# Kernel optimization log

Hardware: AMD Instinct MI355X
Metric: run time of the kernel (lower is better)

## Reference

```python
import math
import jax, jax.numpy as jnp
import numpy as np

EMBED = 1024
INTERNAL = 1024  # EMBED // downsample_rate(=1)
HEADS = 16


def setup_inputs() -> dict:
    key = jax.random.key(0)
    ks = jax.random.split(key, 11)
    b, n, m = 2, 2048, 2048
    s = 1.0 / math.sqrt(EMBED)
    inp = {
        "q": jax.random.normal(ks[0], (b, n, EMBED), jnp.float32),
        "k": jax.random.normal(ks[1], (b, m, EMBED), jnp.float32),
        "v": jax.random.normal(ks[2], (b, m, EMBED), jnp.float32),
        # Linear params (torch Linear: y = x @ W.T + b); store as [in, out].
        "Wq": jax.random.normal(ks[3], (EMBED, INTERNAL), jnp.float32) * s,
        "bq": jax.random.normal(ks[4], (INTERNAL,), jnp.float32) * s,
        "Wk": jax.random.normal(ks[5], (EMBED, INTERNAL), jnp.float32) * s,
        "bk": jax.random.normal(ks[6], (INTERNAL,), jnp.float32) * s,
        "Wv": jax.random.normal(ks[7], (EMBED, INTERNAL), jnp.float32) * s,
        "bv": jax.random.normal(ks[8], (INTERNAL,), jnp.float32) * s,
        "Wo": jax.random.normal(ks[9], (INTERNAL, EMBED), jnp.float32) * s,
        "bo": jax.random.normal(ks[10], (EMBED,), jnp.float32) * s,
    }
    return inp


def _split_heads(x):  # [b, n, c] -> [b, h, n, c/h]
    b, n, c = x.shape
    return x.reshape(b, n, HEADS, c // HEADS).transpose(0, 2, 1, 3)


def reference(q, k, v, Wq, bq, Wk, bk, Wv, bv, Wo, bo):
    qh = _split_heads(q @ Wq + bq)
    kh = _split_heads(k @ Wk + bk)
    vh = _split_heads(v @ Wv + bv)
    c_per_head = kh.shape[-1]
    attn = jnp.einsum("bhnc,bhmc->bhnm", qh, kh) / math.sqrt(c_per_head)
    attn = jax.nn.softmax(attn, axis=-1)
    out = jnp.einsum("bhnm,bhmc->bhnc", attn, vh)
    b, h, n, ch = out.shape
    out = out.transpose(0, 2, 1, 3).reshape(b, n, h * ch)
    return out @ Wo + bo
```

## Files before the change

### kernel.cpp

```cpp
#include <hip/hip_runtime.h>

#define EMBED 1024
#define HEADS 16
#define DHEAD 64
#define BATCH 2
#define SEQ 2048
#define ROWS (BATCH*SEQ)
#define SZA (ROWS*EMBED)
#define SW (EMBED*EMBED)

typedef _Float16 f16;
typedef __attribute__((ext_vector_type(2))) __fp16 h16x2;
typedef __attribute__((ext_vector_type(4))) _Float16 f16x4;
typedef __attribute__((ext_vector_type(8))) _Float16 f16x8;
typedef __attribute__((ext_vector_type(4))) float f32x4;

__device__ __forceinline__ void gld16(const f16* g, f16* lds) {
  __builtin_amdgcn_global_load_lds(
      (const __attribute__((address_space(1))) void*)g,
      (__attribute__((address_space(3))) void*)lds, 16, 0, 0);
}

__global__ __launch_bounds__(256) void pre_kernel(
    const float* __restrict__ q, const float* __restrict__ k,
    const float* __restrict__ v, f16* __restrict__ qc,
    f16* __restrict__ kc, f16* __restrict__ vc,
    const float* __restrict__ w0, const float* __restrict__ w1,
    const float* __restrict__ w2, const float* __restrict__ w3,
    f16* __restrict__ o0, f16* __restrict__ o1,
    f16* __restrict__ o2, f16* __restrict__ o3) {
  __shared__ float tile[32][33];
  const int y = blockIdx.y;
  if (y < 3) {
    const float* in = y == 0 ? q : y == 1 ? k : v;
    f16* out       = y == 0 ? qc : y == 1 ? kc : vc;
    int i = blockIdx.x * 256 + threadIdx.x;
    float4 f = ((const float4* __restrict__)in)[i];
    union { f16 h[4]; short4 s4; } u;
    u.h[0] = (f16)f.x; u.h[1] = (f16)f.y; u.h[2] = (f16)f.z; u.h[3] = (f16)f.w;
    ((short4* __restrict__)out)[i] = u.s4;
    return;
  }
  const int x = blockIdx.x;
  const int z = x >> 10, by = (x >> 5) & 31, bx = x & 31;
  const float* in = z == 0 ? w0 : z == 1 ? w1 : z == 2 ? w2 : w3;
  f16* out       = z == 0 ? o0 : z == 1 ? o1 : z == 2 ? o2 : o3;
  int tx = threadIdx.x & 31, ty = threadIdx.x >> 5;
  #pragma unroll
  for (int i = 0; i < 32; i += 8)
    tile[ty + i][tx] = in[(by*32 + ty + i)*EMBED + bx*32 + tx];
  __syncthreads();
  #pragma unroll
  for (int i = 0; i < 32; i += 8)
    out[(bx*32 + ty + i)*EMBED + by*32 + tx] = (f16)tile[tx][ty + i];
}

__global__ __launch_bounds__(256) void gemm3_kernel(
    const f16* __restrict__ qc, const f16* __restrict__ kc, const f16* __restrict__ vc,
    const f16* __restrict__ Wqt, const f16* __restrict__ Wkt, const f16* __restrict__ Wvt,
    const float* __restrict__ bq, const float* __restrict__ bk, const float* __restrict__ bv,
    f16* __restrict__ Qp, f16* __restrict__ Kp, f16* __restrict__ Vtg) {
  __shared__ __align__(16) f16 As[128*32];
  __shared__ __align__(16) f16 Bs[128*32];
  const int z = blockIdx.y;
  const f16 *A, *Bt; const float* bias; f16* C;
  int mbase, nbase, N, biasrow;
  if (z == 0)      { A=qc;  Bt=Wqt; bias=bq; C=Qp;  mbase=(blockIdx.x&31)*128; nbase=(blockIdx.x>>5)*128; N=EMBED; biasrow=0; }
  else if (z == 1) { A=kc;  Bt=Wkt; bias=bk; C=Kp;  mbase=(blockIdx.x&31)*128; nbase=(blockIdx.x>>5)*128; N=EMBED; biasrow=0; }
  else             { A=Wvt; Bt=vc;  bias=bv; C=Vtg; mbase=(blockIdx.x&7)*128;  nbase=(blockIdx.x>>3)*128; N=ROWS;  biasrow=1; }
  const int K = EMBED;
  const int tid = threadIdx.x;
  const int wave = tid >> 6, lane = tid & 63;
  const int lg = lane >> 4, lr = lane & 15;
  const int wm = (wave >> 1) * 64, wn = (wave & 1) * 64;
  const int sr = lane >> 2;
  const int sc = ((lane & 3) ^ ((lane >> 3) & 3)) * 8;
  const f16* gA0 = A  + (size_t)(mbase + wave*16 + sr)*K + sc;
  const f16* gA1 = A  + (size_t)(mbase + 64 + wave*16 + sr)*K + sc;
  const f16* gB0 = Bt + (size_t)(nbase + wave*16 + sr)*K + sc;
  const f16* gB1 = Bt + (size_t)(nbase + 64 + wave*16 + sr)*K + sc;
  f16* lA0 = &As[(wave*16)*32];
  f16* lA1 = &As[(64 + wave*16)*32];
  f16* lB0 = &Bs[(wave*16)*32];
  f16* lB1 = &Bs[(64 + wave*16)*32];
  const int csw = (lg ^ ((lr >> 1) & 3)) * 8;
  f32x4 acc[4][4] = {};
  for (int k0 = 0; k0 < K; k0 += 32) {
    __syncthreads();
    gld16(gA0 + k0, lA0);
    gld16(gA1 + k0, lA1);
    gld16(gB0 + k0, lB0);
    gld16(gB1 + k0, lB1);
    __syncthreads();
    f16x8 af[4], bf[4];
    #pragma unroll
    for (int mt = 0; mt < 4; mt++)
      af[mt] = *(const f16x8*)&As[(wm + mt*16 + lr)*32 + csw];
    #pragma unroll
    for (int nt = 0; nt < 4; nt++)
      bf[nt] = *(const f16x8*)&Bs[(wn + nt*16 + lr)*32 + csw];
    #pragma unroll
    for (int mt = 0; mt < 4; mt++)
      #pragma unroll
      for (int nt = 0; nt < 4; nt++)
        acc[mt][nt] = __builtin_amdgcn_mfma_f32_16x16x32_f16(af[mt], bf[nt], acc[mt][nt], 0, 0, 0);
  }
  #pragma unroll
  for (int mt = 0; mt < 4; mt++)
    #pragma unroll
    for (int nt = 0; nt < 4; nt++)
      #pragma unroll
      for (int i = 0; i < 4; i++) {
        int row = mbase + wm + mt*16 + lg*4 + i;
        int col = nbase + wn + nt*16 + lr;
        float val = acc[mt][nt][i] + (biasrow ? bias[row] : bias[col]);
        if (z == 0) val *= 0.18033688011f;
        C[(size_t)row*N + col] = (f16)val;
      }
}

__global__ __launch_bounds__(256) void gemmo_kernel(
    const f16* __restrict__ A, const f16* __restrict__ Bt,
    const float* __restrict__ bias, float* __restrict__ Cf) {
  __shared__ __align__(16) f16 As[128*32];
  __shared__ __align__(16) f16 Bs[64*32];
  const int K = EMBED, N = EMBED;
  const int tid = threadIdx.x;
  const int wave = tid >> 6, lane = tid & 63;
  const int lg = lane >> 4, lr = lane & 15;
  const int mbase = blockIdx.x * 128, nbase = blockIdx.y * 64;
  const int wm = (wave >> 1) * 64, wn = (wave & 1) * 32;
  const int sr = wave*16 + (lane >> 2);
  const int sc = ((lane & 3) ^ ((lane >> 3) & 3)) * 8;
  const f16* gA0 = A  + (size_t)(mbase + sr)*K + sc;
  const f16* gA1 = A  + (size_t)(mbase + 64 + sr)*K + sc;
  const f16* gB  = Bt + (size_t)(nbase + sr)*K + sc;
  f16* lA0 = &As[(wave*16)*32];
  f16* lA1 = &As[(64 + wave*16)*32];
  f16* lB  = &Bs[(wave*16)*32];
  const int csw = (lg ^ ((lr >> 1) & 3)) * 8;
  f32x4 acc[4][2] = {};
  for (int k0 = 0; k0 < K; k0 += 32) {
    __syncthreads();
    gld16(gA0 + k0, lA0);
    gld16(gA1 + k0, lA1);
    gld16(gB  + k0, lB);
    __syncthreads();
    f16x8 af[4], bf[2];
    #pragma unroll
    for (int mt = 0; mt < 4; mt++)
      af[mt] = *(const f16x8*)&As[(wm + mt*16 + lr)*32 + csw];
    #pragma unroll
    for (int nt = 0; nt < 2; nt++)
      bf[nt] = *(const f16x8*)&Bs[(wn + nt*16 + lr)*32 + csw];
    #pragma unroll
    for (int mt = 0; mt < 4; mt++)
      #pragma unroll
      for (int nt = 0; nt < 2; nt++)
        acc[mt][nt] = __builtin_amdgcn_mfma_f32_16x16x32_f16(af[mt], bf[nt], acc[mt][nt], 0, 0, 0);
  }
  #pragma unroll
  for (int mt = 0; mt < 4; mt++)
    #pragma unroll
    for (int nt = 0; nt < 2; nt++)
      #pragma unroll
      for (int i = 0; i < 4; i++) {
        int row = mbase + wm + mt*16 + lg*4 + i;
        int col = nbase + wn + nt*16 + lr;
        Cf[(size_t)row*N + col] = acc[mt][nt][i] + bias[col];
      }
}

__global__ __launch_bounds__(256, 1) void attn_kernel(
    const f16* __restrict__ Qp, const f16* __restrict__ Kp,
    const f16* __restrict__ Vt, f16* __restrict__ Ob) {
  __shared__ __align__(16) f16 Ks[2*4096];
  __shared__ __align__(16) f16 Vs[2*4096];
  const int tid = threadIdx.x;
  const int wave = tid >> 6, lane = tid & 63;
  const int lg = lane >> 4, lr = lane & 15;
  const int gid = blockIdx.x;
  const int bh  = (gid & 7)*4 + ((gid >> 3) & 3);
  const int qblk = gid >> 5;
  const int h = bh & 15, b = bh >> 4;
  const int q0 = qblk*256 + wave*64;
  const f16* Qh = Qp + (size_t)b*SEQ*EMBED + h*DHEAD;
  const f16* Kh = Kp + (size_t)b*SEQ*EMBED + h*DHEAD;
  const f16* Vh = Vt + (size_t)h*DHEAD*ROWS + (size_t)b*SEQ;

  const f16* kst[2]; const f16* vst[2]; f16* kdst[2]; f16* vdst[2];
  #pragma unroll
  for (int m = 0; m < 2; m++) {
    int sgrp = m*4 + wave;
    int srow = sgrp*8 + (lane >> 3);
    int sch  = (lane & 7) ^ (srow & 7);
    int prow = ((srow>>5)&1)*32 + ((srow>>4)&1)*4 + ((srow>>2)&3)*8 + (srow&3);
    kst[m] = Kh + (size_t)prow*EMBED + sch*8;
    vst[m] = Vh + (size_t)srow*ROWS + sch*8;
    kdst[m] = &Ks[sgrp*512];
    vdst[m] = &Vs[sgrp*512];
  }

  f16x8 qf[4][2];
  #pragma unroll
  for (int qb = 0; qb < 4; qb++)
    #pragma unroll
    for (int ds = 0; ds < 2; ds++)
      qf[qb][ds] = *(const f16x8*)&Qh[(size_t)(q0 + qb*16 + lr)*EMBED + ds*32 + lg*8];

  const int c0 = ((lg)     ^ (lr & 7)) * 8;
  const int c1 = ((4 + lg) ^ (lr & 7)) * 8;

  f32x4 o[4][4] = {};
  f32x4 lacc[4] = {};
  const f32x4 NEG8 = {-8.f, -8.f, -8.f, -8.f};
  f16x8 onesf;
  #pragma unroll
  for (int i = 0; i < 8; i++) onesf[i] = (f16)1.0f;

  gld16(kst[0], kdst[0]);
  gld16(kst[1], kdst[1]);
  gld16(vst[0], vdst[0]);
  gld16(vst[1], vdst[1]);
  __syncthreads();

  for (int t = 0; t < 32; ++t) {
    const int bo = (t & 1) * 4096;
    if (t < 31) {
      const int po = 4096 - bo;
      const size_t kt = (size_t)(t + 1) * 64;
      gld16(kst[0] + kt*EMBED, kdst[0] + po);
      gld16(kst[1] + kt*EMBED, kdst[1] + po);
      gld16(vst[0] + kt, vdst[0] + po);
      gld16(vst[1] + kt, vdst[1] + po);
    }

    f16x8 ka[4][2], va[4][2];
    #pragma unroll
    for (int nb = 0; nb < 4; nb++) {
      ka[nb][0] = *(const f16x8*)&Ks[bo + (nb*16 + lr)*64 + c0];
      ka[nb][1] = *(const f16x8*)&Ks[bo + (nb*16 + lr)*64 + c1];
    }
    #pragma unroll
    for (int dm = 0; dm < 4; dm++) {
      va[dm][0] = *(const f16x8*)&Vs[bo + (dm*16 + lr)*64 + c0];
      va[dm][1] = *(const f16x8*)&Vs[bo + (dm*16 + lr)*64 + c1];
    }

    #pragma unroll
    for (int qb = 0; qb < 4; qb++) {
      f32x4 s[4];
      __builtin_amdgcn_s_setprio(1);
      #pragma unroll
      for (int nb = 0; nb < 4; nb++) {
        f32x4 z = __builtin_amdgcn_mfma_f32_16x16x32_f16(ka[nb][0], qf[qb][0], NEG8, 0, 0, 0);
        s[nb] = __builtin_amdgcn_mfma_f32_16x16x32_f16(ka[nb][1], qf[qb][1], z, 0, 0, 0);
      }
      __builtin_amdgcn_s_setprio(0);

      float p[4][4];
      #pragma unroll
      for (int nb = 0; nb < 4; nb++)
        #pragma unroll
        for (int i = 0; i < 4; i++)
          p[nb][i] = __builtin_amdgcn_exp2f(s[nb][i]);
      union { f16x8 v; h16x2 h2[4]; } u0, u1;
      u0.h2[0] = __builtin_amdgcn_cvt_pkrtz(p[0][0], p[0][1]);
      u0.h2[1] = __builtin_amdgcn_cvt_pkrtz(p[0][2], p[0][3]);
      u0.h2[2] = __builtin_amdgcn_cvt_pkrtz(p[1][0], p[1][1]);
      u0.h2[3] = __builtin_amdgcn_cvt_pkrtz(p[1][2], p[1][3]);
      u1.h2[0] = __builtin_amdgcn_cvt_pkrtz(p[2][0], p[2][1]);
      u1.h2[1] = __builtin_amdgcn_cvt_pkrtz(p[2][2], p[2][3]);
      u1.h2[2] = __builtin_amdgcn_cvt_pkrtz(p[3][0], p[3][1]);
      u1.h2[3] = __builtin_amdgcn_cvt_pkrtz(p[3][2], p[3][3]);
      const f16x8 pf0 = u0.v, pf1 = u1.v;

      __builtin_amdgcn_s_setprio(1);
      #pragma unroll
      for (int dm = 0; dm < 4; dm++)
        o[dm][qb] = __builtin_amdgcn_mfma_f32_16x16x32_f16(va[dm][0], pf0, o[dm][qb], 0, 0, 0);
      lacc[qb] = __builtin_amdgcn_mfma_f32_16x16x32_f16(onesf, pf0, lacc[qb], 0, 0, 0);
      #pragma unroll
      for (int dm = 0; dm < 4; dm++)
        o[dm][qb] = __builtin_amdgcn_mfma_f32_16x16x32_f16(va[dm][1], pf1, o[dm][qb], 0, 0, 0);
      lacc[qb] = __builtin_amdgcn_mfma_f32_16x16x32_f16(onesf, pf1, lacc[qb], 0, 0, 0);
      __builtin_amdgcn_s_setprio(0);
    }

    __syncthreads();
  }

  const float inv[4] = { 1.f / lacc[0][0], 1.f / lacc[1][0],
                         1.f / lacc[2][0], 1.f / lacc[3][0] };

  #pragma unroll
  for (int qb = 0; qb < 4; qb++) {
    const size_t rowb = (size_t)(b*SEQ + q0 + qb*16 + lr)*EMBED + h*DHEAD;
    #pragma unroll
    for (int dm = 0; dm < 4; dm++) {
      f16x4 w;
      #pragma unroll
      for (int i = 0; i < 4; i++) w[i] = (f16)(o[dm][qb][i] * inv[qb]);
      *(f16x4*)&Ob[rowb + dm*16 + 4*lg] = w;
    }
  }
}

extern "C" void kernel_launch(void* const* d_in, const int* in_sizes, int n_in,
                              void* d_out, int out_size, void* d_ws, size_t ws_size,
                              hipStream_t stream) {
  (void)in_sizes; (void)n_in; (void)out_size; (void)ws_size;
  const float* q  = (const float*)d_in[0];
  const float* k  = (const float*)d_in[1];
  const float* v  = (const float*)d_in[2];
  const float* Wq = (const float*)d_in[3];
  const float* bq = (const float*)d_in[4];
  const float* Wk = (const float*)d_in[5];
  const float* bk = (const float*)d_in[6];
  const float* Wv = (const float*)d_in[7];
  const float* bv = (const float*)d_in[8];
  const float* Wo = (const float*)d_in[9];
  const float* bo = (const float*)d_in[10];
  float* out = (float*)d_out;

  f16* w   = (f16*)d_ws;
  f16* qc  = w;
  f16* kc  = qc + SZA;
  f16* vc  = kc + SZA;
  f16* Qp  = vc + SZA;
  f16* Kp  = Qp + SZA;
  f16* Vtg = Kp + SZA;
  f16* Ob  = Vtg + SZA;
  f16* Wqt = Ob + SZA;
  f16* Wkt = Wqt + SW;
  f16* Wvt = Wkt + SW;
  f16* Wot = Wvt + SW;

  dim3 pg(4096, 4);
  pre_kernel<<<pg, 256, 0, stream>>>(q, k, v, qc, kc, vc,
                                     Wq, Wk, Wv, Wo, Wqt, Wkt, Wvt, Wot);
  dim3 g3(256, 3);
  gemm3_kernel<<<g3, 256, 0, stream>>>(qc, kc, vc, Wqt, Wkt, Wvt, bq, bk, bv, Qp, Kp, Vtg);
  attn_kernel<<<256, 256, 0, stream>>>(Qp, Kp, Vtg, Ob);
  dim3 go(ROWS/128, EMBED/64);
  gemmo_kernel<<<go, 256, 0, stream>>>(Ob, Wot, bo, out);
}
```

Before: 235.6 us.

## Split attention key dimension across wave pairs and double the grid

Each block now covers 128 query rows with four waves, where two waves share each 64-query slab and each handles half of every 64-key tile. Their partial outputs and row sums are combined through shared memory at the end. The grid grows from 256 to 512 blocks and launch bounds allow two blocks per CU, aiming to fill the 256 CUs better and hide latency. The cost is that K/V tiles are loaded twice as often per query, plus an extra reduction step and register pressure limits at two blocks per CU.

Result: faster. 210.7 us (-10.6%).

```diff
diff --git a/kernel.cpp b/kernel.cpp
--- a/kernel.cpp
+++ b/kernel.cpp
@@ -171,19 +171,21 @@
       }
 }
 
-__global__ __launch_bounds__(256, 1) void attn_kernel(
+__global__ __launch_bounds__(256, 2) void attn_kernel(
     const f16* __restrict__ Qp, const f16* __restrict__ Kp,
     const f16* __restrict__ Vt, f16* __restrict__ Ob) {
   __shared__ __align__(16) f16 Ks[2*4096];
   __shared__ __align__(16) f16 Vs[2*4096];
+  __shared__ float lred[2][4][64];
   const int tid = threadIdx.x;
   const int wave = tid >> 6, lane = tid & 63;
   const int lg = lane >> 4, lr = lane & 15;
+  const int qw = wave >> 1, kw = wave & 1;
   const int gid = blockIdx.x;
   const int bh  = (gid & 7)*4 + ((gid >> 3) & 3);
   const int qblk = gid >> 5;
   const int h = bh & 15, b = bh >> 4;
-  const int q0 = qblk*256 + wave*64;
+  const int q0 = qblk*128 + qw*64;
   const f16* Qh = Qp + (size_t)b*SEQ*EMBED + h*DHEAD;
   const f16* Kh = Kp + (size_t)b*SEQ*EMBED + h*DHEAD;
   const f16* Vh = Vt + (size_t)h*DHEAD*ROWS + (size_t)b*SEQ;
@@ -210,6 +212,7 @@
 
   const int c0 = ((lg)     ^ (lr & 7)) * 8;
   const int c1 = ((4 + lg) ^ (lr & 7)) * 8;
+  const int cv = kw ? c1 : c0;
 
   f32x4 o[4][4] = {};
   f32x4 lacc[4] = {};
@@ -224,6 +227,7 @@
   gld16(vst[1], vdst[1]);
   __syncthreads();
 
+  #pragma unroll 2
   for (int t = 0; t < 32; ++t) {
     const int bo = (t & 1) * 4096;
     if (t < 31) {
@@ -235,73 +239,86 @@
       gld16(vst[1] + kt, vdst[1] + po);
     }
 
-    f16x8 ka[4][2], va[4][2];
-    #pragma unroll
-    for (int nb = 0; nb < 4; nb++) {
-      ka[nb][0] = *(const f16x8*)&Ks[bo + (nb*16 + lr)*64 + c0];
-      ka[nb][1] = *(const f16x8*)&Ks[bo + (nb*16 + lr)*64 + c1];
+    f16x8 ka[2][2], va[4];
+    #pragma unroll
+    for (int n = 0; n < 2; n++) {
+      const int nb = 2*kw + n;
+      ka[n][0] = *(const f16x8*)&Ks[bo + (nb*16 + lr)*64 + c0];
+      ka[n][1] = *(const f16x8*)&Ks[bo + (nb*16 + lr)*64 + c1];
     }
     #pragma unroll
-    for (int dm = 0; dm < 4; dm++) {
-      va[dm][0] = *(const f16x8*)&Vs[bo + (dm*16 + lr)*64 + c0];
-      va[dm][1] = *(const f16x8*)&Vs[bo + (dm*16 + lr)*64 + c1];
-    }
+    for (int dm = 0; dm < 4; dm++)
+      va[dm] = *(const f16x8*)&Vs[bo + (dm*16 + lr)*64 + cv];
 
     #pragma unroll
     for (int qb = 0; qb < 4; qb++) {
-      f32x4 s[4];
+      f32x4 s[2];
       __builtin_amdgcn_s_setprio(1);
       #pragma unroll
-      for (int nb = 0; nb < 4; nb++) {
-        f32x4 z = __builtin_amdgcn_mfma_f32_16x16x32_f16(ka[nb][0], qf[qb][0], NEG8, 0, 0, 0);
-        s[nb] = __builtin_amdgcn_mfma_f32_16x16x32_f16(ka[nb][1], qf[qb][1], z, 0, 0, 0);
+      for (int n = 0; n < 2; n++) {
+        f32x4 z = __builtin_amdgcn_mfma_f32_16x16x32_f16(ka[n][0], qf[qb][0], NEG8, 0, 0, 0);
+        s[n] = __builtin_amdgcn_mfma_f32_16x16x32_f16(ka[n][1], qf[qb][1], z, 0, 0, 0);
       }
       __builtin_amdgcn_s_setprio(0);
 
-      float p[4][4];
-      #pragma unroll
-      for (int nb = 0; nb < 4; nb++)
+      float p[2][4];
+      #pragma unroll
+      for (int n = 0; n < 2; n++)
         #pragma unroll
         for (int i = 0; i < 4; i++)
-          p[nb][i] = __builtin_amdgcn_exp2f(s[nb][i]);
-      union { f16x8 v; h16x2 h2[4]; } u0, u1;
-      u0.h2[0] = __builtin_amdgcn_cvt_pkrtz(p[0][0], p[0][1]);
-      u0.h2[1] = __builtin_amdgcn_cvt_pkrtz(p[0][2], p[0][3]);
-      u0.h2[2] = __builtin_amdgcn_cvt_pkrtz(p[1][0], p[1][1]);
-      u0.h2[3] = __builtin_amdgcn_cvt_pkrtz(p[1][2], p[1][3]);
-      u1.h2[0] = __builtin_amdgcn_cvt_pkrtz(p[2][0], p[2][1]);
-      u1.h2[1] = __builtin_amdgcn_cvt_pkrtz(p[2][2], p[2][3]);
-      u1.h2[2] = __builtin_amdgcn_cvt_pkrtz(p[3][0], p[3][1]);
-      u1.h2[3] = __builtin_amdgcn_cvt_pkrtz(p[3][2], p[3][3]);
-      const f16x8 pf0 = u0.v, pf1 = u1.v;
+          p[n][i] = __builtin_amdgcn_exp2f(s[n][i]);
+      union { f16x8 v; h16x2 h2[4]; } u;
+      u.h2[0] = __builtin_amdgcn_cvt_pkrtz(p[0][0], p[0][1]);
+      u.h2[1] = __builtin_amdgcn_cvt_pkrtz(p[0][2], p[0][3]);
+      u.h2[2] = __builtin_amdgcn_cvt_pkrtz(p[1][0], p[1][1]);
+      u.h2[3] = __builtin_amdgcn_cvt_pkrtz(p[1][2], p[1][3]);
+      const f16x8 pf = u.v;
 
       __builtin_amdgcn_s_setprio(1);
       #pragma unroll
       for (int dm = 0; dm < 4; dm++)
-        o[dm][qb] = __builtin_amdgcn_mfma_f32_16x16x32_f16(va[dm][0], pf0, o[dm][qb], 0, 0, 0);
-      lacc[qb] = __builtin_amdgcn_mfma_f32_16x16x32_f16(onesf, pf0, lacc[qb], 0, 0, 0);
-      #pragma unroll
-      for (int dm = 0; dm < 4; dm++)
-        o[dm][qb] = __builtin_amdgcn_mfma_f32_16x16x32_f16(va[dm][1], pf1, o[dm][qb], 0, 0, 0);
-      lacc[qb] = __builtin_amdgcn_mfma_f32_16x16x32_f16(onesf, pf1, lacc[qb], 0, 0, 0);
+        o[dm][qb] = __builtin_amdgcn_mfma_f32_16x16x32_f16(va[dm], pf, o[dm][qb], 0, 0, 0);
+      lacc[qb] = __builtin_amdgcn_mfma_f32_16x16x32_f16(onesf, pf, lacc[qb], 0, 0, 0);
       __builtin_amdgcn_s_setprio(0);
     }
 
     __syncthreads();
   }
 
-  const float inv[4] = { 1.f / lacc[0][0], 1.f / lacc[1][0],
-                         1.f / lacc[2][0], 1.f / lacc[3][0] };
-
-  #pragma unroll
-  for (int qb = 0; qb < 4; qb++) {
-    const size_t rowb = (size_t)(b*SEQ + q0 + qb*16 + lr)*EMBED + h*DHEAD;
-    #pragma unroll
-    for (int dm = 0; dm < 4; dm++) {
-      f16x4 w;
-      #pragma unroll
-      for (int i = 0; i < 4; i++) w[i] = (f16)(o[dm][qb][i] * inv[qb]);
-      *(f16x4*)&Ob[rowb + dm*16 + 4*lg] = w;
+  if (kw == 1) {
+    f32x4* dst = (f32x4*)(qw ? Vs : Ks);
+    #pragma unroll
+    for (int dm = 0; dm < 4; dm++)
+      #pragma unroll
+      for (int qb = 0; qb < 4; qb++)
+        dst[(dm*4 + qb)*64 + lane] = o[dm][qb];
+    #pragma unroll
+    for (int qb = 0; qb < 4; qb++)
+      lred[qw][qb][lane] = lacc[qb][0];
+  }
+  __syncthreads();
+  if (kw == 0) {
+    const f32x4* src = (const f32x4*)(qw ? Vs : Ks);
+    #pragma unroll
+    for (int dm = 0; dm < 4; dm++)
+      #pragma unroll
+      for (int qb = 0; qb < 4; qb++)
+        o[dm][qb] += src[(dm*4 + qb)*64 + lane];
+    float inv[4];
+    #pragma unroll
+    for (int qb = 0; qb < 4; qb++)
+      inv[qb] = 1.f / (lacc[qb][0] + lred[qw][qb][lane]);
+
+    #pragma unroll
+    for (int qb = 0; qb < 4; qb++) {
+      const size_t rowb = (size_t)(b*SEQ + q0 + qb*16 + lr)*EMBED + h*DHEAD;
+      #pragma unroll
+      for (int dm = 0; dm < 4; dm++) {
+        f16x4 w;
+        #pragma unroll
+        for (int i = 0; i < 4; i++) w[i] = (f16)(o[dm][qb][i] * inv[qb]);
+        *(f16x4*)&Ob[rowb + dm*16 + 4*lg] = w;
+      }
     }
   }
 }
@@ -341,7 +358,7 @@
                                      Wq, Wk, Wv, Wo, Wqt, Wkt, Wvt, Wot);
   dim3 g3(256, 3);
   gemm3_kernel<<<g3, 256, 0, stream>>>(qc, kc, vc, Wqt, Wkt, Wvt, bq, bk, bv, Qp, Kp, Vtg);
-  attn_kernel<<<256, 256, 0, stream>>>(Qp, Kp, Vtg, Ob);
+  attn_kernel<<<512, 256, 0, stream>>>(Qp, Kp, Vtg, Ob);
   dim3 go(ROWS/128, EMBED/64);
   gemmo_kernel<<<go, 256, 0, stream>>>(Ob, Wot, bo, out);
 }
```
